# Kernel tuning notes

Measured on AMD Instinct MI355X. Metric: run time of the kernel, lower is better.

Reference implementation:

```python
import jax, jax.numpy as jnp
import numpy as np

K = 16          # nsample (ball-query neighbors via topk smallest sqdist)
EPS = 1e-5      # BatchNorm eps


def conv1(x, W, b):
    # pointwise Conv1d (kernel=1): x [B,N,Cin], W [Cout,Cin], b [Cout] -> [B,N,Cout]
    return jnp.einsum('bnc,oc->bno', x, W) + b


def bn_train(x, gamma, beta):
    # BatchNorm1d in training mode: stats over batch and length dims
    mean = jnp.mean(x, axis=(0, 1))
    var = jnp.var(x, axis=(0, 1))
    return (x - mean) * jax.lax.rsqrt(var + EPS) * gamma + beta


def farthest_point_sample(xyz, npoint):
    # xyz [B,N,3] -> idx [B,npoint]; deterministic start at index 0
    B, N, _ = xyz.shape

    def step(carry, _):
        dist, far = carry                                        # [B,N], [B]
        centroid = jnp.take_along_axis(xyz, far[:, None, None], axis=1)  # [B,1,3]
        d = jnp.sum((xyz - centroid) ** 2, axis=-1)              # [B,N]
        dist = jnp.minimum(dist, d)
        nxt = jnp.argmax(dist, axis=1).astype(jnp.int32)
        return (dist, nxt), far

    init = (jnp.full((B, N), jnp.finfo(xyz.dtype).max, xyz.dtype),
            jnp.zeros((B,), jnp.int32))
    _, idx = jax.lax.scan(step, init, None, length=npoint)       # [npoint,B]
    return idx.T                                                  # [B,npoint]


def sqdist(a, b):
    # a [B,S,3], b [B,N,3] -> [B,S,N]
    return (jnp.sum(a ** 2, -1)[:, :, None]
            + jnp.sum(b ** 2, -1)[:, None, :]
            - 2.0 * jnp.einsum('bsc,bnc->bsn', a, b))


def gather_groups(pc, idx):
    # pc [B,N,D], idx [B,S,K] -> [B,S,K,D]
    return jax.vmap(lambda p, i: p[i])(pc, idx)


def setup_inputs() -> dict:
    key = jax.random.key(0)
    ks = jax.random.split(key, 8)
    B, N = 8, 4096
    mid, out, cin = 32, 64, 3
    s = lambda fan: 1.0 / np.sqrt(fan)
    return {
        'x_in': jax.random.normal(ks[0], (B, N, cin), jnp.float32),
        'W1': jax.random.normal(ks[1], (mid, cin), jnp.float32) * s(cin),
        'b1': jnp.zeros((mid,), jnp.float32),
        'g1': jnp.ones((mid,), jnp.float32),
        'be1': jnp.zeros((mid,), jnp.float32),
        'W2': jax.random.normal(ks[2], (out, mid), jnp.float32) * s(mid),
        'b2': jnp.zeros((out,), jnp.float32),
        'W3': jax.random.normal(ks[3], (out, out + cin), jnp.float32) * s(out + cin),
        'b3': jnp.zeros((out,), jnp.float32),
        'g2': jnp.ones((out,), jnp.float32),
        'be2': jnp.zeros((out,), jnp.float32),
        'W4': jax.random.normal(ks[4], (out, out), jnp.float32) * s(out),
        'b4': jnp.zeros((out,), jnp.float32),
    }


def reference(x_in, W1, b1, g1, be1, W2, b2, W3, b3, g2, be2, W4, b4):
    B, N, C = x_in.shape
    S = N // 2
    # first_mlp: Conv1d -> BN -> ReLU -> Conv1d (all pointwise)
    h = jax.nn.relu(bn_train(conv1(x_in, W1, b1), g1, be1))
    feats = conv1(h, W2, b2)                                  # [B,N,64]
    # sample_and_group(npoint=N//2, nsample=K, xyz=x_in, points=feats)
    fps_idx = farthest_point_sample(x_in, S)                  # [B,S]
    new_xyz = jnp.take_along_axis(x_in, fps_idx[..., None], axis=1)  # [B,S,3]
    d = sqdist(new_xyz, x_in)                                 # [B,S,N]
    _, idx = jax.lax.top_k(-d, K)                             # [B,S,K] smallest dists
    grouped_xyz = gather_groups(x_in, idx) - new_xyz[:, :, None, :]  # [B,S,K,3]
    grouped_pts = gather_groups(feats, idx)                   # [B,S,K,64]
    x_cat = jnp.concatenate([grouped_xyz, grouped_pts], axis=-1)  # [B,S,K,67]
    pooled = jnp.max(x_cat, axis=2)                           # [B,S,67]
    # last_mlp
    h = jax.nn.relu(bn_train(conv1(pooled, W3, b3), g2, be2))
    return conv1(h, W4, b4)                                   # [B,S,64]
```

## Files before the change

kernel.cpp:

```cpp
#include <hip/hip_runtime.h>
#include <float.h>

#define BB   8
#define NN   4096
#define SS   2048
#define MID  32
#define COUT 64
#define CAT  67
#define M1   (BB*NN)
#define M2   (BB*SS)
#define EPSB 1e-5f
#define NCHUNK 64
#define CSZ    32

#define WI_CTR   0
#define WI_TKT   4
#define WI_PROG  8
#define WS_RED2  32
#define WS_RED1  160
#define WS_FPS   1024
#define WS_FEATS (1024 + 16384)
#define WS_POOL  (WS_FEATS + M1*COUT)

struct SA  { float red[8][9]; };
struct SB4 { float4 Pc[NN]; alignas(16) unsigned long long sv[2][8]; };
struct SB3 { float W1s[96]; float abv[64]; float W2s[2048]; float b2s[64]; float mom[9]; };
struct SC  { float4 Pq[NN]; unsigned long long cand[CSZ][257]; int fin[CSZ][16]; int tkt; };
struct SC2 { float W3s[64 * CAT]; float b3s[64]; float ps[128]; };
struct SE  { float W3t[CAT * 64]; float W4s[4096]; float b3s[64]; float b4s[64]; float ab[128]; };
union  SU  { SA a; SB4 b4; SB3 b3; SC c; SC2 c2; SE e; };

__device__ __forceinline__ unsigned long long u64max(unsigned long long a,
                                                     unsigned long long b) {
    return a > b ? a : b;
}

template <int CTRL>
__device__ __forceinline__ unsigned long long dpp_swap_max(unsigned long long v) {
    int lo = (int)(unsigned)v;
    int hi = (int)(unsigned)(v >> 32);
    int olo = __builtin_amdgcn_update_dpp(0, lo, CTRL, 0xF, 0xF, false);
    int ohi = __builtin_amdgcn_update_dpp(0, hi, CTRL, 0xF, 0xF, false);
    unsigned long long ov = ((unsigned long long)(unsigned)ohi << 32) | (unsigned)olo;
    return u64max(v, ov);
}

__device__ __forceinline__ void barrier_join(int* ctr, int target) {
    __syncthreads();
    if (threadIdx.x == 0) {
        __threadfence();
        atomicAdd(ctr, 1);
        while (atomicAdd(ctr, 0) < target) __builtin_amdgcn_s_sleep(16);
        __threadfence();
    }
    __syncthreads();
}

__device__ __forceinline__ void top16_insert(unsigned long long* cv,
                                             unsigned long long newv,
                                             unsigned long long& cmaxv, int& cpos) {
#pragma unroll
    for (int j = 0; j < 16; j++) cv[j] = (j == cpos) ? newv : cv[j];
    unsigned long long m1a[8]; int p1a[8];
#pragma unroll
    for (int j = 0; j < 8; j++) {
        bool s = cv[2 * j + 1] > cv[2 * j];
        m1a[j] = s ? cv[2 * j + 1] : cv[2 * j];
        p1a[j] = s ? 2 * j + 1 : 2 * j;
    }
    unsigned long long m2a[4]; int p2a[4];
#pragma unroll
    for (int j = 0; j < 4; j++) {
        bool s = m1a[2 * j + 1] > m1a[2 * j];
        m2a[j] = s ? m1a[2 * j + 1] : m1a[2 * j];
        p2a[j] = s ? p1a[2 * j + 1] : p1a[2 * j];
    }
    unsigned long long m3a, m3b; int p3a, p3b;
    { bool s = m2a[1] > m2a[0]; m3a = s ? m2a[1] : m2a[0]; p3a = s ? p2a[1] : p2a[0]; }
    { bool s = m2a[3] > m2a[2]; m3b = s ? m2a[3] : m2a[2]; p3b = s ? p2a[3] : p2a[2]; }
    bool s = m3b > m3a;
    cmaxv = s ? m3b : m3a; cpos = s ? p3b : p3a;
}

__global__ __launch_bounds__(512) void fused(
        const float* __restrict__ xin,
        const float* __restrict__ W1, const float* __restrict__ b1,
        const float* __restrict__ g1, const float* __restrict__ be1,
        const float* __restrict__ W2, const float* __restrict__ b2,
        const float* __restrict__ W3, const float* __restrict__ b3,
        const float* __restrict__ g2, const float* __restrict__ be2,
        const float* __restrict__ W4, const float* __restrict__ b4,
        float* __restrict__ ws, float* __restrict__ out) {
    __shared__ SU sm;
    int blk = blockIdx.x, tid = threadIdx.x;
    int* ctri  = (int*)ws;
    int* prog  = ctri + WI_PROG;
    int* fidxg = (int*)(ws + WS_FPS);
    (void)b1;

    if (blk < 8) {
        int b = blk;
        const float* xb = xin + (size_t)b * NN * 3;
        float px[8], py[8], pz[8], dist[8];
#pragma unroll
        for (int k = 0; k < 8; k++) {
            int i = tid + (k << 9);
            float x = xb[3 * i], y = xb[3 * i + 1], z = xb[3 * i + 2];
            px[k] = x; py[k] = y; pz[k] = z; dist[k] = FLT_MAX;
            sm.b4.Pc[i] = make_float4(x, y, z, 0.f);
        }
        if (tid == 0)
            __hip_atomic_store(fidxg + b * SS, 0, __ATOMIC_RELAXED, __HIP_MEMORY_SCOPE_AGENT);
        __syncthreads();
        float4 c0 = sm.b4.Pc[0];
        float cx = c0.x, cy = c0.y, cz = c0.z;
        int wid = tid >> 6, lane = tid & 63;
        for (int t = 1; t < SS; t++) {
            float bv = -1.f; int bi = 0;
#pragma unroll
            for (int k = 0; k < 8; k++) {
                float dx = px[k] - cx, dy = py[k] - cy, dz = pz[k] - cz;
                float d = fmaf(dz, dz, fmaf(dy, dy, dx * dx));
                float nd = fminf(dist[k], d);
                dist[k] = nd;
                bool bt = nd > bv;
                bv = bt ? nd : bv; bi = bt ? (tid + (k << 9)) : bi;
            }
            unsigned long long v =
                ((unsigned long long)__float_as_uint(bv) << 32) | (unsigned)(~bi);
            v = dpp_swap_max<0xB1>(v);
            v = dpp_swap_max<0x4E>(v);
            v = dpp_swap_max<0x141>(v);
            v = dpp_swap_max<0x140>(v);
            {
                int a16 = ((lane ^ 16) << 2), a32 = ((lane ^ 32) << 2), a48 = ((lane ^ 48) << 2);
                int lo = (int)(unsigned)v, hi = (int)(unsigned)(v >> 32);
                int lo16 = __builtin_amdgcn_ds_bpermute(a16, lo);
                int hi16 = __builtin_amdgcn_ds_bpermute(a16, hi);
                int lo32 = __builtin_amdgcn_ds_bpermute(a32, lo);
                int hi32 = __builtin_amdgcn_ds_bpermute(a32, hi);
                int lo48 = __builtin_amdgcn_ds_bpermute(a48, lo);
                int hi48 = __builtin_amdgcn_ds_bpermute(a48, hi);
                unsigned long long v16 = ((unsigned long long)(unsigned)hi16 << 32) | (unsigned)lo16;
                unsigned long long v32 = ((unsigned long long)(unsigned)hi32 << 32) | (unsigned)lo32;
                unsigned long long v48 = ((unsigned long long)(unsigned)hi48 << 32) | (unsigned)lo48;
                v = u64max(u64max(v, v16), u64max(v32, v48));
            }
            int par = t & 1;
            if (lane == 0) sm.b4.sv[par][wid] = v;
            __syncthreads();
            const ulonglong2* sp = (const ulonglong2*)sm.b4.sv[par];
            ulonglong2 q0 = sp[0], q1 = sp[1], q2 = sp[2], q3 = sp[3];
            unsigned long long m0 = u64max(q0.x, q0.y), m1 = u64max(q1.x, q1.y);
            unsigned long long m2 = u64max(q2.x, q2.y), m3 = u64max(q3.x, q3.y);
            unsigned long long best = u64max(u64max(m0, m1), u64max(m2, m3));
            int bsel = (int)(~(unsigned)best);
            float4 cc = sm.b4.Pc[bsel];
            cx = cc.x; cy = cc.y; cz = cc.z;
            if (tid == 0) {
                __hip_atomic_store(fidxg + b * SS + t, bsel,
                                   __ATOMIC_RELAXED, __HIP_MEMORY_SCOPE_AGENT);
                if (((t + 1) & (CSZ - 1)) == 0)
                    __hip_atomic_store(prog + b, t + 1,
                                       __ATOMIC_RELEASE, __HIP_MEMORY_SCOPE_AGENT);
            }
        }
        barrier_join(ctri + 2, 256);
    } else {
        if (blk < 72) {
            int p = (blk - 8) * 512 + tid;
            float x0 = xin[3 * p], x1 = xin[3 * p + 1], x2 = xin[3 * p + 2];
            float r[9];
            r[0] = x0; r[1] = x1; r[2] = x2;
            r[3] = x0 * x0; r[4] = x0 * x1; r[5] = x0 * x2;
            r[6] = x1 * x1; r[7] = x1 * x2; r[8] = x2 * x2;
#pragma unroll
            for (int m = 32; m; m >>= 1) {
#pragma unroll
                for (int q = 0; q < 9; q++) r[q] += __shfl_down(r[q], m, 64);
            }
            if ((tid & 63) == 0) {
#pragma unroll
                for (int q = 0; q < 9; q++) sm.a.red[tid >> 6][q] = r[q];
            }
            __syncthreads();
            if (tid == 0) {
#pragma unroll
                for (int q = 0; q < 9; q++) {
                    float s = 0.f;
#pragma unroll
                    for (int w = 0; w < 8; w++) s += sm.a.red[w][q];
                    ws[WS_RED1 + (blk - 8) * 9 + q] = s;
                }
            }
            barrier_join(ctri + 0, 64);
            for (int j = tid; j < 96; j += 512) sm.b3.W1s[j] = W1[j];
            if (tid < 64) sm.b3.b2s[tid] = b2[tid];
            for (int j = tid; j < 2048; j += 512) sm.b3.W2s[j] = W2[j];
            if (tid < 9) {
                float s = 0.f;
                for (int k = 0; k < 64; k++) s += ws[WS_RED1 + k * 9 + tid];
                sm.b3.mom[tid] = s;
            }
            __syncthreads();
            if (tid < MID) {
                float S0 = sm.b3.mom[0], S1 = sm.b3.mom[1], S2 = sm.b3.mom[2];
                float C00 = sm.b3.mom[3], C01 = sm.b3.mom[4], C02 = sm.b3.mom[5];
                float C11 = sm.b3.mom[6], C12 = sm.b3.mom[7], C22 = sm.b3.mom[8];
                float w0 = W1[3 * tid], w1 = W1[3 * tid + 1], w2 = W1[3 * tid + 2];
                float invM = 1.f / (float)M1;
                float meanc = (w0 * S0 + w1 * S1 + w2 * S2) * invM;
                float wCw = w0 * w0 * C00 + w1 * w1 * C11 + w2 * w2 * C22 +
                            2.f * (w0 * w1 * C01 + w0 * w2 * C02 + w1 * w2 * C12);
                float var = wCw * invM - meanc * meanc;
                float a = g1[tid] * rsqrtf(var + EPSB);
                sm.b3.abv[tid] = a;
                sm.b3.abv[MID + tid] = be1[tid] - meanc * a;
            }
            __syncthreads();
            int p2 = (blk - 8) * 512 + tid;
            float y0 = xin[3 * p2], y1 = xin[3 * p2 + 1], y2 = xin[3 * p2 + 2];
            float h[MID];
#pragma unroll
            for (int o = 0; o < MID; o++) {
                float y = fmaf(sm.b3.W1s[3 * o + 2], y2,
                         fmaf(sm.b3.W1s[3 * o + 1], y1, sm.b3.W1s[3 * o] * y0));
                h[o] = fmaxf(0.f, fmaf(sm.b3.abv[o], y, sm.b3.abv[MID + o]));
            }
            float* fo = ws + WS_FEATS + (size_t)p2 * COUT;
#pragma unroll
            for (int j = 0; j < COUT; j += 4) {
                float a0 = sm.b3.b2s[j], a1v = sm.b3.b2s[j + 1];
                float a2v = sm.b3.b2s[j + 2], a3v = sm.b3.b2s[j + 3];
#pragma unroll
                for (int o = 0; o < MID; o++) {
                    float hv = h[o];
                    a0  = fmaf(sm.b3.W2s[(j)     * MID + o], hv, a0);
                    a1v = fmaf(sm.b3.W2s[(j + 1) * MID + o], hv, a1v);
                    a2v = fmaf(sm.b3.W2s[(j + 2) * MID + o], hv, a2v);
                    a3v = fmaf(sm.b3.W2s[(j + 3) * MID + o], hv, a3v);
                }
                *(float4*)(fo + j) = make_float4(a0, a1v, a2v, a3v);
            }
        }
        barrier_join(ctri + 1, 248);

        int curb = -1;
        for (;;) {
            if (tid == 0) sm.c.tkt = atomicAdd(ctri + WI_TKT, 1);
            __syncthreads();
            int tk = sm.c.tkt;
            if (tk >= BB * NCHUNK) break;
            int b = tk & 7, c = tk >> 3;
            if (b != curb) {
                const float* xb = xin + (size_t)b * NN * 3;
                for (int j = tid; j < NN; j += 512) {
                    float x = xb[3 * j], y = xb[3 * j + 1], z = xb[3 * j + 2];
                    sm.c.Pq[j] = make_float4(x, y, z, (x * x + y * y) + z * z);
                }
                curb = b;
            }
            if (tid == 0) {
                int need = (c + 1) * CSZ;
                while (__hip_atomic_load(prog + b, __ATOMIC_ACQUIRE,
                                         __HIP_MEMORY_SCOPE_AGENT) < need)
                    __builtin_amdgcn_s_sleep(8);
            }
            __syncthreads();
            int cc = tid >> 4, q = tid & 15;
            int s = c * CSZ + cc;
            int sg = b * SS + s;
            int ci = __hip_atomic_load(fidxg + sg, __ATOMIC_RELAXED,
                                       __HIP_MEMORY_SCOPE_AGENT);
            float4 cen = sm.c.Pq[ci];
            float an = cen.w;
            unsigned long long cv[16];
#pragma unroll
            for (int j = 0; j < 16; j++) cv[j] = ~0ULL;
            unsigned long long cmaxv = ~0ULL; int cpos = 0;
            for (int n0 = 0; n0 < 256; n0++) {
                int n = (q << 8) + ((n0 + q) & 255);
                float4 qq = sm.c.Pq[n];
                float dot = fmaf(cen.z, qq.z, fmaf(cen.y, qq.y, cen.x * qq.x));
                float dd = (an + qq.w) - 2.f * dot;
                unsigned db = __float_as_uint(dd);
                db ^= (unsigned)(((int)db >> 31) | 0x80000000u);
                unsigned long long newv = ((unsigned long long)db << 32) | (unsigned)n;
                if (newv < cmaxv) top16_insert(cv, newv, cmaxv, cpos);
            }
#pragma unroll
            for (int j = 0; j < 16; j++) sm.c.cand[cc][q * 16 + j] = cv[j];
            __syncthreads();
            if (tid < CSZ) {
                unsigned long long mv[16];
#pragma unroll
                for (int j = 0; j < 16; j++) mv[j] = ~0ULL;
                unsigned long long mx = ~0ULL; int mp = 0;
                for (int k = 0; k < 256; k++) {
                    unsigned long long e = sm.c.cand[tid][k];
                    if (e < mx) top16_insert(mv, e, mx, mp);
                }
#pragma unroll
                for (int j = 0; j < 16; j++) sm.c.fin[tid][j] = (int)(unsigned)mv[j];
            }
            __syncthreads();
            int idxs[16];
#pragma unroll
            for (int j = 0; j < 16; j++) idxs[j] = sm.c.fin[cc][j];
            const float* feats = ws + WS_FEATS + (size_t)b * NN * COUT;
            float4 acc = make_float4(-FLT_MAX, -FLT_MAX, -FLT_MAX, -FLT_MAX);
#pragma unroll 4
            for (int k = 0; k < 16; k++) {
                const float4* fp = (const float4*)(feats + (size_t)idxs[k] * COUT) + q;
                float4 v0 = fp[0];
                acc.x = fmaxf(acc.x, v0.x); acc.y = fmaxf(acc.y, v0.y);
                acc.z = fmaxf(acc.z, v0.z); acc.w = fmaxf(acc.w, v0.w);
            }
            float* po = ws + WS_POOL + (size_t)sg * CAT;
            po[3 + q * 4] = acc.x; po[4 + q * 4] = acc.y;
            po[5 + q * 4] = acc.z; po[6 + q * 4] = acc.w;
            if (q == 0) {
                float rx = -FLT_MAX, ry = -FLT_MAX, rz = -FLT_MAX;
#pragma unroll
                for (int k = 0; k < 16; k++) {
                    float4 p = sm.c.Pq[idxs[k]];
                    rx = fmaxf(rx, p.x - cen.x);
                    ry = fmaxf(ry, p.y - cen.y);
                    rz = fmaxf(rz, p.z - cen.z);
                }
                po[0] = rx; po[1] = ry; po[2] = rz;
            }
        }
        barrier_join(ctri + 2, 256);
    }

    {
        for (int j = tid; j < 64 * CAT; j += 512) sm.c2.W3s[j] = W3[j];
        if (tid < 64) sm.c2.b3s[tid] = b3[tid];
        if (tid < 128) sm.c2.ps[tid] = 0.f;
        __syncthreads();
        int cch = tid & 63, g = tid >> 6;
        float sum = 0.f, sq = 0.f;
        for (int m = 0; m < 8; m++) {
            int row = blk * 64 + g * 8 + m;
            const float* r = ws + WS_POOL + (size_t)row * CAT;
            float y = sm.c2.b3s[cch];
            for (int j = 0; j < CAT; j++) y = fmaf(sm.c2.W3s[cch * CAT + j], r[j], y);
            sum += y; sq = fmaf(y, y, sq);
        }
        atomicAdd(&sm.c2.ps[cch], sum);
        atomicAdd(&sm.c2.ps[64 + cch], sq);
        __syncthreads();
        if (tid < 128) atomicAdd(ws + WS_RED2 + tid, sm.c2.ps[tid]);
    }
    barrier_join(ctri + 3, 256);

    {
        for (int lin = tid; lin < CAT * 64; lin += 512) {
            int j = lin >> 6, o = lin & 63;
            sm.e.W3t[lin] = W3[o * CAT + j];
        }
        for (int j = tid; j < 4096; j += 512) sm.e.W4s[j] = W4[j];
        if (tid < 64) {
            sm.e.b3s[tid] = b3[tid]; sm.e.b4s[tid] = b4[tid];
            float inv = 1.f / (float)M2;
            float mean = ws[WS_RED2 + tid] * inv;
            float var = ws[WS_RED2 + 64 + tid] * inv - mean * mean;
            float a = g2[tid] * rsqrtf(var + EPSB);
            sm.e.ab[tid] = a;
            sm.e.ab[64 + tid] = be2[tid] - mean * a;
        }
        __syncthreads();
        if (tid < 64) {
            int pt = blk * 64 + tid;
            const float* row = ws + WS_POOL + (size_t)pt * CAT;
            float h[64];
#pragma unroll
            for (int c = 0; c < 64; c++) h[c] = sm.e.b3s[c];
            for (int j = 0; j < CAT; j++) {
                float pj = row[j];
#pragma unroll
                for (int c = 0; c < 64; c++) h[c] = fmaf(sm.e.W3t[j * 64 + c], pj, h[c]);
            }
#pragma unroll
            for (int c = 0; c < 64; c++)
                h[c] = fmaxf(0.f, fmaf(sm.e.ab[c], h[c], sm.e.ab[64 + c]));
            float* op = out + (size_t)pt * 64;
            for (int o = 0; o < 64; o += 4) {
                float a0 = sm.e.b4s[o], a1v = sm.e.b4s[o + 1];
                float a2v = sm.e.b4s[o + 2], a3v = sm.e.b4s[o + 3];
#pragma unroll
                for (int c = 0; c < 64; c++) {
                    float hv = h[c];
                    a0  = fmaf(sm.e.W4s[(o)     * 64 + c], hv, a0);
                    a1v = fmaf(sm.e.W4s[(o + 1) * 64 + c], hv, a1v);
                    a2v = fmaf(sm.e.W4s[(o + 2) * 64 + c], hv, a2v);
                    a3v = fmaf(sm.e.W4s[(o + 3) * 64 + c], hv, a3v);
                }
                *(float4*)(op + o) = make_float4(a0, a1v, a2v, a3v);
            }
        }
    }
}

extern "C" void kernel_launch(void* const* d_in, const int* in_sizes, int n_in,
                              void* d_out, int out_size, void* d_ws, size_t ws_size,
                              hipStream_t stream) {
    (void)in_sizes; (void)n_in; (void)out_size; (void)ws_size;
    const float* xin = (const float*)d_in[0];
    const float* W1  = (const float*)d_in[1];
    const float* b1  = (const float*)d_in[2];
    const float* g1  = (const float*)d_in[3];
    const float* be1 = (const float*)d_in[4];
    const float* W2  = (const float*)d_in[5];
    const float* b2  = (const float*)d_in[6];
    const float* W3  = (const float*)d_in[7];
    const float* b3  = (const float*)d_in[8];
    const float* g2  = (const float*)d_in[9];
    const float* be2 = (const float*)d_in[10];
    const float* W4  = (const float*)d_in[11];
    const float* b4  = (const float*)d_in[12];
    float* ws  = (float*)d_ws;
    float* out = (float*)d_out;

    hipMemsetAsync(d_ws, 0, 4096, stream);
    void* args[] = {
        (void*)&xin, (void*)&W1, (void*)&b1, (void*)&g1, (void*)&be1,
        (void*)&W2, (void*)&b2, (void*)&W3, (void*)&b3, (void*)&g2,
        (void*)&be2, (void*)&W4, (void*)&b4, (void*)&ws, (void*)&out
    };
    hipLaunchCooperativeKernel((const void*)fused, dim3(256), dim3(512),
                               args, 0, stream);
}
```

Baseline: 2.182 ms.

## Fuse BN2 statistics into grouping workers and drop a grid barrier

Worker blocks now compute the W3 conv and the per-channel sum and sum-of-squares for each chunk right after pooling it. This removes the separate stats phase and one grid-wide barrier. The FPS blocks now write indices in batched int4 stores, and progress counters and barrier counters sit on separate padded slots. Spin loops use relaxed loads with longer sleeps. The FPS blocks no longer take part in the stats reduction, and index 0 relies on the buffered write.

```diff
diff --git a/kernel.cpp b/kernel.cpp
--- a/kernel.cpp
+++ b/kernel.cpp
@@ -13,11 +13,13 @@
 #define NCHUNK 64
 #define CSZ    32
 
-#define WI_CTR   0
-#define WI_TKT   4
-#define WI_PROG  8
-#define WS_RED2  32
-#define WS_RED1  160
+#define I_B0   0
+#define I_B1   16
+#define I_B2   32
+#define I_TKT  64
+#define I_PROG 80
+#define WS_RED2  256
+#define WS_RED1  400
 #define WS_FPS   1024
 #define WS_FEATS (1024 + 16384)
 #define WS_POOL  (WS_FEATS + M1*COUT)
@@ -25,10 +27,10 @@
 struct SA  { float red[8][9]; };
 struct SB4 { float4 Pc[NN]; alignas(16) unsigned long long sv[2][8]; };
 struct SB3 { float W1s[96]; float abv[64]; float W2s[2048]; float b2s[64]; float mom[9]; };
-struct SC  { float4 Pq[NN]; unsigned long long cand[CSZ][257]; int fin[CSZ][16]; int tkt; };
-struct SC2 { float W3s[64 * CAT]; float b3s[64]; float ps[128]; };
+struct SC  { float4 Pq[NN]; unsigned long long cand[CSZ][257]; int fin[CSZ][16];
+             float W3s[64 * CAT]; float b3s[64]; float ps[128]; int tkt; };
 struct SE  { float W3t[CAT * 64]; float W4s[4096]; float b3s[64]; float b4s[64]; float ab[128]; };
-union  SU  { SA a; SB4 b4; SB3 b3; SC c; SC2 c2; SE e; };
+union  SU  { SA a; SB4 b4; SB3 b3; SC c; SE e; };
 
 __device__ __forceinline__ unsigned long long u64max(unsigned long long a,
                                                      unsigned long long b) {
@@ -50,7 +52,8 @@
     if (threadIdx.x == 0) {
         __threadfence();
         atomicAdd(ctr, 1);
-        while (atomicAdd(ctr, 0) < target) __builtin_amdgcn_s_sleep(16);
+        while (__hip_atomic_load(ctr, __ATOMIC_RELAXED, __HIP_MEMORY_SCOPE_AGENT) < target)
+            __builtin_amdgcn_s_sleep(64);
         __threadfence();
     }
     __syncthreads();
@@ -94,13 +97,14 @@
     __shared__ SU sm;
     int blk = blockIdx.x, tid = threadIdx.x;
     int* ctri  = (int*)ws;
-    int* prog  = ctri + WI_PROG;
     int* fidxg = (int*)(ws + WS_FPS);
     (void)b1;
 
     if (blk < 8) {
         int b = blk;
         const float* xb = xin + (size_t)b * NN * 3;
+        int* fob = fidxg + b * SS;
+        int* progb = ctri + I_PROG + b * 16;
         float px[8], py[8], pz[8], dist[8];
 #pragma unroll
         for (int k = 0; k < 8; k++) {
@@ -109,12 +113,12 @@
             px[k] = x; py[k] = y; pz[k] = z; dist[k] = FLT_MAX;
             sm.b4.Pc[i] = make_float4(x, y, z, 0.f);
         }
-        if (tid == 0)
-            __hip_atomic_store(fidxg + b * SS, 0, __ATOMIC_RELAXED, __HIP_MEMORY_SCOPE_AGENT);
         __syncthreads();
         float4 c0 = sm.b4.Pc[0];
         float cx = c0.x, cy = c0.y, cz = c0.z;
         int wid = tid >> 6, lane = tid & 63;
+        int rbuf[8];
+        rbuf[0] = 0;
         for (int t = 1; t < SS; t++) {
             float bv = -1.f; int bi = 0;
 #pragma unroll
@@ -158,14 +162,17 @@
             float4 cc = sm.b4.Pc[bsel];
             cx = cc.x; cy = cc.y; cz = cc.z;
             if (tid == 0) {
-                __hip_atomic_store(fidxg + b * SS + t, bsel,
-                                   __ATOMIC_RELAXED, __HIP_MEMORY_SCOPE_AGENT);
-                if (((t + 1) & (CSZ - 1)) == 0)
-                    __hip_atomic_store(prog + b, t + 1,
-                                       __ATOMIC_RELEASE, __HIP_MEMORY_SCOPE_AGENT);
-            }
-        }
-        barrier_join(ctri + 2, 256);
+                rbuf[t & 7] = bsel;
+                if ((t & 7) == 7) {
+                    *(int4*)(fob + t - 7) = make_int4(rbuf[0], rbuf[1], rbuf[2], rbuf[3]);
+                    *(int4*)(fob + t - 3) = make_int4(rbuf[4], rbuf[5], rbuf[6], rbuf[7]);
+                    if ((t & 31) == 31)
+                        __hip_atomic_store(progb, t + 1, __ATOMIC_RELEASE,
+                                           __HIP_MEMORY_SCOPE_AGENT);
+                }
+            }
+        }
+        barrier_join(ctri + I_B2, 256);
     } else {
         if (blk < 72) {
             int p = (blk - 8) * 512 + tid;
@@ -193,7 +200,7 @@
                     ws[WS_RED1 + (blk - 8) * 9 + q] = s;
                 }
             }
-            barrier_join(ctri + 0, 64);
+            barrier_join(ctri + I_B0, 64);
             for (int j = tid; j < 96; j += 512) sm.b3.W1s[j] = W1[j];
             if (tid < 64) sm.b3.b2s[tid] = b2[tid];
             for (int j = tid; j < 2048; j += 512) sm.b3.W2s[j] = W2[j];
@@ -243,11 +250,17 @@
                 *(float4*)(fo + j) = make_float4(a0, a1v, a2v, a3v);
             }
         }
-        barrier_join(ctri + 1, 248);
-
+        barrier_join(ctri + I_B1, 248);
+
+        for (int j = tid; j < 64 * CAT; j += 512) sm.c.W3s[j] = W3[j];
+        if (tid < 64) sm.c.b3s[tid] = b3[tid];
+        if (tid < 128) sm.c.ps[tid] = 0.f;
+        __syncthreads();
+        int c0ch = (tid & 15) * 4;
+        float bsum[4] = {0.f, 0.f, 0.f, 0.f}, bsq[4] = {0.f, 0.f, 0.f, 0.f};
         int curb = -1;
         for (;;) {
-            if (tid == 0) sm.c.tkt = atomicAdd(ctri + WI_TKT, 1);
+            if (tid == 0) sm.c.tkt = atomicAdd(ctri + I_TKT, 1);
             __syncthreads();
             int tk = sm.c.tkt;
             if (tk >= BB * NCHUNK) break;
@@ -261,17 +274,19 @@
                 curb = b;
             }
             if (tid == 0) {
+                int* progb = ctri + I_PROG + b * 16;
                 int need = (c + 1) * CSZ;
-                while (__hip_atomic_load(prog + b, __ATOMIC_ACQUIRE,
+                while (__hip_atomic_load(progb, __ATOMIC_RELAXED,
                                          __HIP_MEMORY_SCOPE_AGENT) < need)
-                    __builtin_amdgcn_s_sleep(8);
+                    __builtin_amdgcn_s_sleep(64);
+                (void)__hip_atomic_load(progb, __ATOMIC_ACQUIRE,
+                                        __HIP_MEMORY_SCOPE_AGENT);
             }
             __syncthreads();
             int cc = tid >> 4, q = tid & 15;
             int s = c * CSZ + cc;
             int sg = b * SS + s;
-            int ci = __hip_atomic_load(fidxg + sg, __ATOMIC_RELAXED,
-                                       __HIP_MEMORY_SCOPE_AGENT);
+            int ci = fidxg[sg];
             float4 cen = sm.c.Pq[ci];
             float an = cen.w;
             unsigned long long cv[16];
@@ -330,30 +345,34 @@
                 }
                 po[0] = rx; po[1] = ry; po[2] = rz;
             }
-        }
-        barrier_join(ctri + 2, 256);
+            __syncthreads();
+            {
+                int rrow = b * SS + c * CSZ + (tid >> 4);
+                const float* rp = ws + WS_POOL + (size_t)rrow * CAT;
+                float y0 = sm.c.b3s[c0ch],     y1 = sm.c.b3s[c0ch + 1];
+                float y2 = sm.c.b3s[c0ch + 2], y3 = sm.c.b3s[c0ch + 3];
+                for (int j = 0; j < CAT; j++) {
+                    float pj = rp[j];
+                    y0 = fmaf(sm.c.W3s[(c0ch)     * CAT + j], pj, y0);
+                    y1 = fmaf(sm.c.W3s[(c0ch + 1) * CAT + j], pj, y1);
+                    y2 = fmaf(sm.c.W3s[(c0ch + 2) * CAT + j], pj, y2);
+                    y3 = fmaf(sm.c.W3s[(c0ch + 3) * CAT + j], pj, y3);
+                }
+                bsum[0] += y0; bsq[0] = fmaf(y0, y0, bsq[0]);
+                bsum[1] += y1; bsq[1] = fmaf(y1, y1, bsq[1]);
+                bsum[2] += y2; bsq[2] = fmaf(y2, y2, bsq[2]);
+                bsum[3] += y3; bsq[3] = fmaf(y3, y3, bsq[3]);
+            }
+        }
+#pragma unroll
+        for (int u = 0; u < 4; u++) {
+            atomicAdd(&sm.c.ps[c0ch + u], bsum[u]);
+            atomicAdd(&sm.c.ps[64 + c0ch + u], bsq[u]);
+        }
+        __syncthreads();
+        if (tid < 128) atomicAdd(ws + WS_RED2 + tid, sm.c.ps[tid]);
+        barrier_join(ctri + I_B2, 256);
     }
-
-    {
-        for (int j = tid; j < 64 * CAT; j += 512) sm.c2.W3s[j] = W3[j];
-        if (tid < 64) sm.c2.b3s[tid] = b3[tid];
-        if (tid < 128) sm.c2.ps[tid] = 0.f;
-        __syncthreads();
-        int cch = tid & 63, g = tid >> 6;
-        float sum = 0.f, sq = 0.f;
-        for (int m = 0; m < 8; m++) {
-            int row = blk * 64 + g * 8 + m;
-            const float* r = ws + WS_POOL + (size_t)row * CAT;
-            float y = sm.c2.b3s[cch];
-            for (int j = 0; j < CAT; j++) y = fmaf(sm.c2.W3s[cch * CAT + j], r[j], y);
-            sum += y; sq = fmaf(y, y, sq);
-        }
-        atomicAdd(&sm.c2.ps[cch], sum);
-        atomicAdd(&sm.c2.ps[64 + cch], sq);
-        __syncthreads();
-        if (tid < 128) atomicAdd(ws + WS_RED2 + tid, sm.c2.ps[tid]);
-    }
-    barrier_join(ctri + 3, 256);
 
     {
         for (int lin = tid; lin < CAT * 64; lin += 512) {
```

New measurement: 2.097 ms. 3.9% less time.
